# Kernel tuning notes

Measured on AMD Instinct MI355X. Metric: run time of the kernel, lower is better.

Reference implementation:

```python
import jax, jax.numpy as jnp
import numpy as np

GRID_H = 128
GRID_W = 128
N_POS = 8192
RAD = 1.5
EPS = 1e-12


def setup_inputs() -> dict:
    key = jax.random.key(0)
    k_pos, k_maze = jax.random.split(key)
    # positions uniformly spread over the maze extent [0, H] x [0, W]
    pos = jax.random.uniform(k_pos, (N_POS, 2), dtype=jnp.float32)
    pos = pos * jnp.array([GRID_H, GRID_W], dtype=jnp.float32)
    maze = (jax.random.uniform(k_maze, (GRID_H, GRID_W)) < 0.3).astype(jnp.float32)
    rad = jnp.float32(RAD)
    return {"pos": pos, "maze": maze, "rad": rad}


def reference(pos, maze, rad):
    # pos:  [N, 2] query positions
    # maze: [H, W] occupancy grid (1.0 = wall cell)
    # rad:  scalar collision radius
    H, W = maze.shape
    # cell centers at (i + 0.5, j + 0.5)
    ii = jnp.arange(H, dtype=pos.dtype) + 0.5
    jj = jnp.arange(W, dtype=pos.dtype) + 0.5
    ci, cj = jnp.meshgrid(ii, jj, indexing="ij")
    centers = jnp.stack([ci.ravel(), cj.ravel()], axis=-1)  # [M, 2], M = H*W
    occ = maze.ravel()                                       # [M]
    # squared distances via ||p||^2 + ||c||^2 - 2 p.c  (avoids [N, M, 2] diff tensor)
    p2 = jnp.sum(pos * pos, axis=-1, keepdims=True)          # [N, 1]
    c2 = jnp.sum(centers * centers, axis=-1)                 # [M]
    d2 = p2 + c2 - 2.0 * jnp.einsum("nd,md->nm", pos, centers)  # [N, M]
    d = jnp.sqrt(jnp.maximum(d2, EPS))
    # penetration penalty within collision radius, weighted by occupancy
    pen = jax.nn.relu(rad - d) * occ                         # [N, M]
    count = jnp.sum(pen)
    return count
```

## Files before the change

kernel.cpp:

```cpp
#include <hip/hip_runtime.h>

#define GRID_H 128
#define GRID_W 128
#define N_POS  8192
#define NBLOCKS 8
#define NTHREADS 1024
#define EPS_F  1e-12f
#define MAGIC  0x5CA1AB1Eu

__global__ __launch_bounds__(NTHREADS) void MazeCollision_kernel(
    const float* __restrict__ pos,
    const float* __restrict__ maze,
    const float* __restrict__ rad_p,
    float* __restrict__ out,
    float* __restrict__ vals,
    unsigned int* __restrict__ flags)
{
    const int t = threadIdx.x;
    const int bid = blockIdx.x;
    const float rad = rad_p[0];

    const int gid = bid * NTHREADS + t;
    const float2 xy = ((const float2*)pos)[gid];
    const float x = xy.x, y = xy.y;

    float acc = 0.0f;
    if (rad <= 1.5f) {
        const int i0 = (int)floorf(x) - 1;
        const int j0 = (int)floorf(y) - 1;
        float dy2[4], colm[4];
        int jc[4];
        #pragma unroll
        for (int c = 0; c < 4; ++c) {
            const int j = j0 + c;
            const float dy = y - ((float)j + 0.5f);
            dy2[c] = dy * dy;
            colm[c] = ((unsigned)j < GRID_W) ? 1.0f : 0.0f;
            jc[c] = min(max(j, 0), GRID_W - 1);
        }
        #pragma unroll
        for (int r = 0; r < 4; ++r) {
            const int i = i0 + r;
            const float rowm = ((unsigned)i < GRID_H) ? 1.0f : 0.0f;
            const int ic = min(max(i, 0), GRID_H - 1);
            const float dx = x - ((float)i + 0.5f);
            const float dx2 = dx * dx;
            const int rowbase = ic * GRID_W;
            #pragma unroll
            for (int c = 0; c < 4; ++c) {
                const float occ = maze[rowbase + jc[c]];
                const float d = __builtin_amdgcn_sqrtf(fmaxf(dx2 + dy2[c], EPS_F));
                const float pen = fmaxf(rad - d, 0.0f);
                acc += pen * occ * (rowm * colm[c]);
            }
        }
    } else {
        const int ilo = max(0, (int)floorf(x - 0.5f - rad));
        const int ihi = min(GRID_H - 1, (int)ceilf(x - 0.5f + rad));
        const int jlo = max(0, (int)floorf(y - 0.5f - rad));
        const int jhi = min(GRID_W - 1, (int)ceilf(y - 0.5f + rad));
        for (int i = ilo; i <= ihi; ++i) {
            const float dx = x - ((float)i + 0.5f);
            const float dx2 = dx * dx;
            for (int j = jlo; j <= jhi; ++j) {
                const float dyv = y - ((float)j + 0.5f);
                const float d = sqrtf(fmaxf(dx2 + dyv * dyv, EPS_F));
                acc += fmaxf(rad - d, 0.0f) * maze[i * GRID_W + j];
            }
        }
    }

    #pragma unroll
    for (int off = 32; off > 0; off >>= 1)
        acc += __shfl_down(acc, off, 64);

    __shared__ float wsum[NTHREADS / 64];
    if ((t & 63) == 0) wsum[t >> 6] = acc;
    __syncthreads();

    if (t < NTHREADS / 64) {
        float v = wsum[t];
        #pragma unroll
        for (int off = 8; off > 0; off >>= 1)
            v += __shfl_down(v, off, 64);

        if (bid != 0) {
            if (t == 0) {
                __hip_atomic_store(&vals[bid], v, __ATOMIC_RELAXED, __HIP_MEMORY_SCOPE_AGENT);
                __hip_atomic_store(&flags[bid], MAGIC, __ATOMIC_RELEASE, __HIP_MEMORY_SCOPE_AGENT);
            }
        } else {
            float g = 0.0f;
            if (t == 0) g = v;
            if (t >= 1 && t < NBLOCKS) {
                while (__hip_atomic_load(&flags[t], __ATOMIC_ACQUIRE, __HIP_MEMORY_SCOPE_AGENT) != MAGIC) {}
                g = __hip_atomic_load(&vals[t], __ATOMIC_RELAXED, __HIP_MEMORY_SCOPE_AGENT);
                __hip_atomic_store(&flags[t], 0u, __ATOMIC_RELAXED, __HIP_MEMORY_SCOPE_AGENT);
            }
            #pragma unroll
            for (int off = 4; off > 0; off >>= 1)
                g += __shfl_down(g, off, 64);
            if (t == 0) out[0] = g;
        }
    }
}

extern "C" void kernel_launch(void* const* d_in, const int* in_sizes, int n_in,
                              void* d_out, int out_size, void* d_ws, size_t ws_size,
                              hipStream_t stream) {
    const float* pos  = (const float*)d_in[0];
    const float* maze = (const float*)d_in[1];
    const float* rad  = (const float*)d_in[2];
    float* out = (float*)d_out;
    float* vals = (float*)d_ws;
    unsigned int* flags = (unsigned int*)((char*)d_ws + 256);

    MazeCollision_kernel<<<NBLOCKS, NTHREADS, 0, stream>>>(pos, maze, rad, out, vals, flags);
}
```

Baseline: 11.88 us.

## Stage maze in LDS and shrink collision stencil to clamped 3x3

Each block copies the whole 128x128 occupancy grid into shared memory with float4 loads, then reads occupancy from LDS instead of gathering scattered global loads. The per-position stencil drops from 4x4 to 3x3 cells. The window is clamped to stay inside the grid, which removes the per-cell bounds masks. This trades scattered dependent global gathers for a 64KB bulk copy per block plus a barrier, and the large LDS allocation limits how many blocks can share a CU.

```diff
diff --git a/kernel.cpp b/kernel.cpp
--- a/kernel.cpp
+++ b/kernel.cpp
@@ -16,42 +16,42 @@
     float* __restrict__ vals,
     unsigned int* __restrict__ flags)
 {
+    __shared__ float smaze[GRID_H * GRID_W];
     const int t = threadIdx.x;
     const int bid = blockIdx.x;
+
+    {
+        const float4* m4 = (const float4*)maze;
+        float4* s4 = (float4*)smaze;
+        #pragma unroll
+        for (int k = 0; k < (GRID_H * GRID_W / 4) / NTHREADS; ++k)
+            s4[t + k * NTHREADS] = m4[t + k * NTHREADS];
+    }
     const float rad = rad_p[0];
-
-    const int gid = bid * NTHREADS + t;
-    const float2 xy = ((const float2*)pos)[gid];
+    const float2 xy = ((const float2*)pos)[bid * NTHREADS + t];
     const float x = xy.x, y = xy.y;
+    __syncthreads();
 
     float acc = 0.0f;
     if (rad <= 1.5f) {
-        const int i0 = (int)floorf(x) - 1;
-        const int j0 = (int)floorf(y) - 1;
-        float dy2[4], colm[4];
-        int jc[4];
+        const int i0 = min(max((int)floorf(x) - 1, 0), GRID_H - 3);
+        const int j0 = min(max((int)floorf(y) - 1, 0), GRID_W - 3);
+        float dy2[3];
         #pragma unroll
-        for (int c = 0; c < 4; ++c) {
-            const int j = j0 + c;
-            const float dy = y - ((float)j + 0.5f);
+        for (int c = 0; c < 3; ++c) {
+            const float dy = y - ((float)(j0 + c) + 0.5f);
             dy2[c] = dy * dy;
-            colm[c] = ((unsigned)j < GRID_W) ? 1.0f : 0.0f;
-            jc[c] = min(max(j, 0), GRID_W - 1);
         }
+        const int base = i0 * GRID_W + j0;
         #pragma unroll
-        for (int r = 0; r < 4; ++r) {
-            const int i = i0 + r;
-            const float rowm = ((unsigned)i < GRID_H) ? 1.0f : 0.0f;
-            const int ic = min(max(i, 0), GRID_H - 1);
-            const float dx = x - ((float)i + 0.5f);
+        for (int r = 0; r < 3; ++r) {
+            const float dx = x - ((float)(i0 + r) + 0.5f);
             const float dx2 = dx * dx;
-            const int rowbase = ic * GRID_W;
             #pragma unroll
-            for (int c = 0; c < 4; ++c) {
-                const float occ = maze[rowbase + jc[c]];
+            for (int c = 0; c < 3; ++c) {
+                const float occ = smaze[base + r * GRID_W + c];
                 const float d = __builtin_amdgcn_sqrtf(fmaxf(dx2 + dy2[c], EPS_F));
-                const float pen = fmaxf(rad - d, 0.0f);
-                acc += pen * occ * (rowm * colm[c]);
+                acc += fmaxf(rad - d, 0.0f) * occ;
             }
         }
     } else {
@@ -65,7 +65,7 @@
             for (int j = jlo; j <= jhi; ++j) {
                 const float dyv = y - ((float)j + 0.5f);
                 const float d = sqrtf(fmaxf(dx2 + dyv * dyv, EPS_F));
-                acc += fmaxf(rad - d, 0.0f) * maze[i * GRID_W + j];
+                acc += fmaxf(rad - d, 0.0f) * smaze[i * GRID_W + j];
             }
         }
     }
```

Result: slower. 14.06 us (+18.4%).
